# Performance work log

Measured on AMD Instinct MI355X. Metric: run time of the kernel, lower is better.

Reference implementation:

```python
import jax, jax.numpy as jnp
import numpy as np

EMB = 512
HEADS = 8
WINDOW = 128


def setup_inputs() -> dict:
    key = jax.random.key(0)
    ks = jax.random.split(key, 9)
    s = 1.0 / np.sqrt(EMB)
    x = jax.random.normal(ks[0], (2, 4096, EMB), dtype=jnp.float32)
    mk = lambda k: jax.random.uniform(k, (EMB, EMB), jnp.float32, -s, s)
    mb = lambda k: jax.random.uniform(k, (EMB,), jnp.float32, -s, s)
    return {
        "x": x,
        "Wq": mk(ks[1]), "bq": mb(ks[2]),
        "Wk": mk(ks[3]), "bk": mb(ks[4]),
        "Wv": mk(ks[5]), "bv": mb(ks[6]),
        "Wo": mk(ks[7]), "bo": mb(ks[8]),
    }


def _split_heads(y, b, n):
    # [b, n, emb] -> [b, h, n, d]
    return y.reshape(b, n, HEADS, EMB // HEADS).transpose(0, 2, 1, 3)


def reference(x, Wq, bq, Wk, bk, Wv, bv, Wo, bo):
    b, n, _ = x.shape
    q = _split_heads(x @ Wq.T + bq, b, n)
    k = _split_heads(x @ Wk.T + bk, b, n)
    v = _split_heads(x @ Wv.T + bv, b, n)
    energy = jnp.einsum('bhqd,bhkd->bhqk', q, k)  # [b,h,n,n]
    idx = jnp.arange(n)
    # banded mask: disallowed where |i - j| > window (matches torch loop)
    disallow = jnp.abs(idx[:, None] - idx[None, :]) > WINDOW
    fmin = jnp.float32(np.finfo(np.float32).min)
    energy = jnp.where(disallow[None, None], fmin, energy)
    att = jax.nn.softmax(energy / jnp.float32(np.sqrt(EMB)), axis=-1)
    out = jnp.einsum('bhql,bhld->bhqd', att, v)
    out = out.transpose(0, 2, 1, 3).reshape(b, n, EMB)
    return out @ Wo.T + bo
```

## Files before the change

### kernel.cpp

```cpp
#include <hip/hip_runtime.h>

#define EMB 512
#define HEADS 8
#define HD 64
#define NSEQ 4096
#define BATCH 2
#define WINDOW 128

typedef unsigned short u16;
typedef __attribute__((ext_vector_type(8))) short bf16x8;
typedef __attribute__((ext_vector_type(4))) float f32x4;

#define XS 4194304u
#define WS 262144u
#define BS 512u

__device__ __forceinline__ float bf2f(u16 u) {
    union { unsigned int i; float f; } x;
    x.i = ((unsigned int)u) << 16;
    return x.f;
}

__device__ __forceinline__ u16 f2bf(float f) {
    union { float f; unsigned int i; } x;
    x.f = f;
    unsigned int i = x.i;
    unsigned int lsb = (i >> 16) & 1u;
    i += 0x7fffu + lsb;
    return (u16)(i >> 16);
}

struct raw8 { uint4 lo, hi; };

__device__ __forceinline__ raw8 loadraw8(const void* base, size_t off, int isbf) {
    raw8 r;
    if (isbf) {
        r.lo = *(const uint4*)((const u16*)base + off);
    } else {
        const float* f = (const float*)base + off;
        r.lo = *(const uint4*)f;
        r.hi = *(const uint4*)(f + 4);
    }
    return r;
}

__device__ __forceinline__ uint4 cvt8(const raw8& r, int isbf) {
    if (isbf) return r.lo;
    const float* a = (const float*)&r.lo;
    const float* b = (const float*)&r.hi;
    uint4 o;
    o.x = (unsigned)f2bf(a[0]) | ((unsigned)f2bf(a[1]) << 16);
    o.y = (unsigned)f2bf(a[2]) | ((unsigned)f2bf(a[3]) << 16);
    o.z = (unsigned)f2bf(b[0]) | ((unsigned)f2bf(b[1]) << 16);
    o.w = (unsigned)f2bf(b[2]) | ((unsigned)f2bf(b[3]) << 16);
    return o;
}

__device__ __forceinline__ int probe_bf16(const void* p) {
    const int lane = threadIdx.x & 63;
    u16 w = ((const u16*)p)[lane * 2];
    int e = (w >> 7) & 0xff;
    bool sane = (w == 0) || (e >= 100 && e <= 140);
    unsigned long long m = __ballot(sane);
    return __popcll(m) >= 48;
}

__global__ __launch_bounds__(256)
void prepass(const void* __restrict__ x,
             const void* __restrict__ Wq, const void* __restrict__ bq,
             const void* __restrict__ Wk, const void* __restrict__ bk,
             const void* __restrict__ Wv, const void* __restrict__ bv,
             const void* __restrict__ Wo, const void* __restrict__ bo,
             u16* __restrict__ xb, u16* __restrict__ wb, u16* __restrict__ bb,
             int* __restrict__ flags)
{
    const int fx  = probe_bf16(x);
    const int fwq = probe_bf16(Wq), fbq = probe_bf16(bq);
    const int fwk = probe_bf16(Wk), fbk = probe_bf16(bk);
    const int fwv = probe_bf16(Wv), fbv = probe_bf16(bv);
    const int fwo = probe_bf16(Wo), fbo = probe_bf16(bo);
    if (blockIdx.x == 0 && threadIdx.x == 0) flags[0] = fx;

    size_t idx = ((size_t)blockIdx.x * 256 + threadIdx.x) * 8;
    const size_t T_X = XS, T_W = XS + 4 * (size_t)WS, T_ALL = T_W + 4 * (size_t)BS;
    if (idx >= T_ALL) return;

    const void* src; int fl; u16* dst; size_t off;
    if (idx < T_X) {
        src = x; fl = fx; dst = xb; off = idx;
    } else if (idx < T_W) {
        size_t w = idx - T_X;
        int wi = (int)(w / WS); off = w % WS;
        src = (wi == 0) ? Wq : (wi == 1) ? Wk : (wi == 2) ? Wv : Wo;
        fl  = (wi == 0) ? fwq : (wi == 1) ? fwk : (wi == 2) ? fwv : fwo;
        dst = wb + (size_t)wi * WS;
    } else {
        size_t b = idx - T_W;
        int bi = (int)(b / BS); off = b % BS;
        src = (bi == 0) ? bq : (bi == 1) ? bk : (bi == 2) ? bv : bo;
        fl  = (bi == 0) ? fbq : (bi == 1) ? fbk : (bi == 2) ? fbv : fbo;
        dst = bb + (size_t)bi * BS;
    }
    *(uint4*)(dst + off) = cvt8(loadraw8(src, off, fl), fl);
}

__global__ __launch_bounds__(256)
void qkv_gemm(const u16* __restrict__ X, const u16* __restrict__ Wall,
              const u16* __restrict__ ball,
              u16* __restrict__ qo, u16* __restrict__ ko, u16* __restrict__ vo)
{
    __shared__ __align__(16) u16 As2[2][128 * 32];
    __shared__ __align__(16) u16 Bs2[2][128 * 32];

    const int tid  = threadIdx.x;
    const int wave = tid >> 6;
    const int lane = tid & 63;
    const int quad = lane >> 4;
    const int l16  = lane & 15;
    const int wm = wave >> 1, wn = wave & 1;

    const int m0 = blockIdx.x * 128;
    const int by = blockIdx.y;
    const int wsel = by >> 2;
    const int n0 = (by & 3) * 128;

    const u16* W  = Wall + (size_t)wsel * WS;
    const u16* bi = ball + (size_t)wsel * BS;
    const float oscale = (wsel == 0) ? 0.04419417382415922f : 1.0f;

    const u16* PA = (wsel == 2) ? W : X;
    const u16* PB = (wsel == 2) ? X : W;
    const int abase = (wsel == 2) ? n0 : m0;
    const int bbase = (wsel == 2) ? m0 : n0;

    f32x4 acc[4][4];
#pragma unroll
    for (int i = 0; i < 4; ++i)
#pragma unroll
        for (int j = 0; j < 4; ++j)
            acc[i][j] = (f32x4){0.f, 0.f, 0.f, 0.f};

    const int c1 = tid, c2 = tid + 256;
    const int r1 = c1 >> 2, k1 = (c1 & 3) * 8;
    const int r2 = c2 >> 2, k2 = (c2 & 3) * 8;

    uint4 a1 = *(const uint4*)(PA + (size_t)(abase + r1) * EMB + k1);
    uint4 a2 = *(const uint4*)(PA + (size_t)(abase + r2) * EMB + k2);
    uint4 b1 = *(const uint4*)(PB + (size_t)(bbase + r1) * EMB + k1);
    uint4 b2 = *(const uint4*)(PB + (size_t)(bbase + r2) * EMB + k2);
    *(uint4*)&As2[0][c1 * 8] = a1;
    *(uint4*)&As2[0][c2 * 8] = a2;
    *(uint4*)&Bs2[0][c1 * 8] = b1;
    *(uint4*)&Bs2[0][c2 * 8] = b2;
    a1 = *(const uint4*)(PA + (size_t)(abase + r1) * EMB + 32 + k1);
    a2 = *(const uint4*)(PA + (size_t)(abase + r2) * EMB + 32 + k2);
    b1 = *(const uint4*)(PB + (size_t)(bbase + r1) * EMB + 32 + k1);
    b2 = *(const uint4*)(PB + (size_t)(bbase + r2) * EMB + 32 + k2);
    __syncthreads();

    for (int kt = 0; kt < 16; ++kt) {
        const int cur = kt & 1;

        bf16x8 af[4], bfr[4];
#pragma unroll
        for (int i = 0; i < 4; ++i)
            af[i] = *(const bf16x8*)&As2[cur][(wm * 64 + i * 16 + l16) * 32 + quad * 8];
#pragma unroll
        for (int j = 0; j < 4; ++j)
            bfr[j] = *(const bf16x8*)&Bs2[cur][(wn * 64 + j * 16 + l16) * 32 + quad * 8];

        if (kt < 15) {
            *(uint4*)&As2[cur ^ 1][c1 * 8] = a1;
            *(uint4*)&As2[cur ^ 1][c2 * 8] = a2;
            *(uint4*)&Bs2[cur ^ 1][c1 * 8] = b1;
            *(uint4*)&Bs2[cur ^ 1][c2 * 8] = b2;
        }
        if (kt < 14) {
            const int kk0 = (kt + 2) * 32;
            a1 = *(const uint4*)(PA + (size_t)(abase + r1) * EMB + kk0 + k1);
            a2 = *(const uint4*)(PA + (size_t)(abase + r2) * EMB + kk0 + k2);
            b1 = *(const uint4*)(PB + (size_t)(bbase + r1) * EMB + kk0 + k1);
            b2 = *(const uint4*)(PB + (size_t)(bbase + r2) * EMB + kk0 + k2);
        }

#pragma unroll
        for (int i = 0; i < 4; ++i)
#pragma unroll
            for (int j = 0; j < 4; ++j)
                acc[i][j] = __builtin_amdgcn_mfma_f32_16x16x32_bf16(af[i], bfr[j], acc[i][j], 0, 0, 0);

        if (kt < 15) __syncthreads();
    }

    if (wsel != 2) {
#pragma unroll
        for (int j = 0; j < 4; ++j) {
            const int col = n0 + wn * 64 + j * 16 + l16;
            const float bv_ = bf2f(bi[col]);
            const int h = col >> 6, d = col & 63;
            u16* out = (wsel == 0) ? qo : ko;
#pragma unroll
            for (int i = 0; i < 4; ++i) {
#pragma unroll
                for (int r = 0; r < 4; ++r) {
                    const int row = m0 + wm * 64 + i * 16 + quad * 4 + r;
                    const int b = row >> 12, n = row & 4095;
                    out[(((size_t)(b * HEADS + h) * NSEQ) + n) * HD + d] =
                        f2bf((acc[i][j][r] + bv_) * oscale);
                }
            }
        }
    } else {
#pragma unroll
        for (int i = 0; i < 4; ++i) {
#pragma unroll
            for (int r = 0; r < 4; ++r) {
                const int dglob = n0 + wm * 64 + i * 16 + quad * 4 + r;
                const float bv_ = bf2f(bi[dglob]);
                const int h = dglob >> 6, dd = dglob & 63;
#pragma unroll
                for (int j = 0; j < 4; ++j) {
                    const int ncol = m0 + wn * 64 + j * 16 + l16;
                    const int b = ncol >> 12, n = ncol & 4095;
                    vo[((size_t)(b * HEADS + h) * HD + dd) * NSEQ + n] =
                        f2bf(acc[i][j][r] + bv_);
                }
            }
        }
    }
}

#define KP 72
#define VP 72
__global__ __launch_bounds__(256)
void attn_mfma(const u16* __restrict__ q, const u16* __restrict__ k,
               const u16* __restrict__ vt, u16* __restrict__ ao)
{
    __shared__ __align__(16) u16 Ks2[2][64 * KP];
    __shared__ __align__(16) u16 Vt2[2][64 * VP];
    __shared__ __align__(16) u16 Vones[16 * VP];
    __shared__ __align__(16) u16 Pb[4][16 * KP];

    const int tid  = threadIdx.x;
    const int wave = tid >> 6;
    const int lane = tid & 63;
    const int quad = lane >> 4;
    const int l16  = lane & 15;

    int wg = blockIdx.y * 64 + blockIdx.x;
    wg = (wg & 7) * 128 + (wg >> 3);
    const int bh = wg >> 6;
    const int q0 = (wg & 63) * 64;

    const int qw = q0 + wave * 16;
    const size_t base = (size_t)bh * NSEQ * HD;
    const bool interior = (q0 >= 128) && (q0 <= NSEQ - 192);

    if (tid < VP) {
        Vones[tid] = (u16)0x3f80;
#pragma unroll
        for (int rr = 1; rr < 16; ++rr) Vones[rr * VP + tid] = 0;
    }

    bf16x8 qa0 = *(const bf16x8*)(q + base + (size_t)(qw + l16) * HD + quad * 8);
    bf16x8 qa1 = *(const bf16x8*)(q + base + (size_t)(qw + l16) * HD + 32 + quad * 8);

    f32x4 O[4], O4;
#pragma unroll
    for (int t = 0; t < 4; ++t) O[t] = (f32x4){0.f, 0.f, 0.f, 0.f};
    O4 = (f32x4){0.f, 0.f, 0.f, 0.f};

    const int key_s[2] = { tid >> 3, (tid + 256) >> 3 };
    const int ch8      = (tid & 7) * 8;

    const int pacol = (quad * 8) ^ ((l16 >> 2) << 4);

    uint4 pkv[2], pvv[2];
#pragma unroll
    for (int s = 0; s < 2; ++s) {
        int kg = q0 - 128 + key_s[s];
        kg = (kg < 0) ? 0 : (kg > NSEQ - 1 ? NSEQ - 1 : kg);
        pkv[s] = *(const uint4*)(k + base + (size_t)kg * HD + ch8);
        int kc = q0 - 128 + ch8;
        kc = (kc < 0) ? 0 : (kc > NSEQ - 8 ? NSEQ - 8 : kc);
        pvv[s] = *(const uint4*)(vt + base + (size_t)key_s[s] * NSEQ + kc);
    }
#pragma unroll
    for (int s = 0; s < 2; ++s) {
        *(uint4*)&Ks2[0][key_s[s] * KP + ch8] = pkv[s];
        *(uint4*)&Vt2[0][key_s[s] * VP + ch8] = pvv[s];
    }
#pragma unroll
    for (int s = 0; s < 2; ++s) {
        int kg = q0 - 64 + key_s[s];
        kg = (kg < 0) ? 0 : (kg > NSEQ - 1 ? NSEQ - 1 : kg);
        pkv[s] = *(const uint4*)(k + base + (size_t)kg * HD + ch8);
        int kc = q0 - 64 + ch8;
        kc = (kc < 0) ? 0 : (kc > NSEQ - 8 ? NSEQ - 8 : kc);
        pvv[s] = *(const uint4*)(vt + base + (size_t)key_s[s] * NSEQ + kc);
    }
    __syncthreads();

    for (int c = 0; c < 5; ++c) {
        const int cur = c & 1;
        const int kbase = q0 - 128 + c * 64;

        if (c < 4) {
#pragma unroll
            for (int s = 0; s < 2; ++s) {
                *(uint4*)&Ks2[cur ^ 1][key_s[s] * KP + ch8] = pkv[s];
                *(uint4*)&Vt2[cur ^ 1][key_s[s] * VP + ch8] = pvv[s];
            }
        }
        if (c < 3) {
            const int nb = kbase + 128;
#pragma unroll
            for (int s = 0; s < 2; ++s) {
                int kg = nb + key_s[s];
                kg = (kg < 0) ? 0 : (kg > NSEQ - 1 ? NSEQ - 1 : kg);
                pkv[s] = *(const uint4*)(k + base + (size_t)kg * HD + ch8);
                int kc = nb + ch8;
                kc = (kc < 0) ? 0 : (kc > NSEQ - 8 ? NSEQ - 8 : kc);
                pvv[s] = *(const uint4*)(vt + base + (size_t)key_s[s] * NSEQ + kc);
            }
        }

        const int gdk = kbase - qw;
        const bool act = (gdk <= 143) && (gdk >= -191) &&
                         (kbase > -64) && (kbase < NSEQ);
        if (act) {
            f32x4 sv[4];
#pragma unroll
            for (int t = 0; t < 4; ++t) {
                const int dk = gdk + t * 16;
                if (dk >= -143 && dk <= 143) {
                    bf16x8 b0 = *(const bf16x8*)&Ks2[cur][(t * 16 + l16) * KP + quad * 8];
                    bf16x8 b1 = *(const bf16x8*)&Ks2[cur][(t * 16 + l16) * KP + 32 + quad * 8];
                    f32x4 sacc = (f32x4){0.f, 0.f, 0.f, 0.f};
                    sacc = __builtin_amdgcn_mfma_f32_16x16x32_bf16(qa0, b0, sacc, 0, 0, 0);
                    sacc = __builtin_amdgcn_mfma_f32_16x16x32_bf16(qa1, b1, sacc, 0, 0, 0);
                    if (!interior || dk < -113 || dk > 113) {
                        const int jg = kbase + t * 16 + l16;
                        const bool jok = ((unsigned)jg) < (unsigned)NSEQ;
#pragma unroll
                        for (int r = 0; r < 4; ++r) {
                            const int iq = qw + quad * 4 + r;
                            const bool band = ((unsigned)(iq - jg + WINDOW)) <= (unsigned)(2 * WINDOW);
                            if (!(jok && band)) sacc[r] = -1e30f;
                        }
                    }
                    sv[t] = sacc;
                } else {
                    sv[t] = (f32x4){-1e30f, -1e30f, -1e30f, -1e30f};
                }
            }

#pragma unroll
            for (int t = 0; t < 4; ++t) {
                const int tc = (t ^ quad) * 16 + l16;
#pragma unroll
                for (int r = 0; r < 4; ++r) {
                    const float pv = __expf(fminf(sv[t][r], 40.f));
                    Pb[wave][(quad * 4 + r) * KP + tc] = f2bf(pv);
                }
            }

#pragma unroll
            for (int ks2 = 0; ks2 < 2; ++ks2) {
                bf16x8 pa = *(const bf16x8*)&Pb[wave][l16 * KP + (pacol ^ (ks2 * 32))];
#pragma unroll
                for (int t = 0; t < 4; ++t) {
                    bf16x8 vb = *(const bf16x8*)&Vt2[cur][(t * 16 + l16) * VP + ks2 * 32 + quad * 8];
                    O[t] = __builtin_amdgcn_mfma_f32_16x16x32_bf16(pa, vb, O[t], 0, 0, 0);
                }
                bf16x8 vb4 = *(const bf16x8*)&Vones[l16 * VP + ks2 * 32 + quad * 8];
                O4 = __builtin_amdgcn_mfma_f32_16x16x32_bf16(pa, vb4, O4, 0, 0, 0);
            }
        }

        if (c < 4) __syncthreads();
    }

    const int bb = bh >> 3, hh = bh & 7;
    float rl[4];
#pragma unroll
    for (int r = 0; r < 4; ++r) {
        const float ls = __shfl(O4[r], lane & 48, 64);
        rl[r] = 1.f / ls;
    }
#pragma unroll
    for (int t = 0; t < 4; ++t)
#pragma unroll
        for (int r = 0; r < 4; ++r) {
            const int iq = qw + quad * 4 + r;
            ao[((size_t)(bb * NSEQ + iq)) * EMB + hh * HD + t * 16 + l16] =
                f2bf(O[t][r] * rl[r]);
        }
}

__global__ __launch_bounds__(256)
void out_gemm(const u16* __restrict__ A, const u16* __restrict__ W,
              const u16* __restrict__ bias, void* __restrict__ out,
              const int* __restrict__ flags)
{
    __shared__ __align__(16) u16 As2[2][128 * 32];
    __shared__ __align__(16) u16 Bs2[2][128 * 32];

    const int tid  = threadIdx.x;
    const int wave = tid >> 6;
    const int lane = tid & 63;
    const int quad = lane >> 4;
    const int l16  = lane & 15;
    const int wm = wave >> 1, wn = wave & 1;

    const int m0 = blockIdx.x * 128;
    const int n0 = blockIdx.y * 128;
    const int fo = flags[0];

    f32x4 acc[4][4];
#pragma unroll
    for (int i = 0; i < 4; ++i)
#pragma unroll
        for (int j = 0; j < 4; ++j)
            acc[i][j] = (f32x4){0.f, 0.f, 0.f, 0.f};

    const int c1 = tid, c2 = tid + 256;
    const int r1 = c1 >> 2, k1 = (c1 & 3) * 8;
    const int r2 = c2 >> 2, k2 = (c2 & 3) * 8;

    uint4 a1 = *(const uint4*)(A + (size_t)(m0 + r1) * EMB + k1);
    uint4 a2 = *(const uint4*)(A + (size_t)(m0 + r2) * EMB + k2);
    uint4 b1 = *(const uint4*)(W + (size_t)(n0 + r1) * EMB + k1);
    uint4 b2 = *(const uint4*)(W + (size_t)(n0 + r2) * EMB + k2);
    *(uint4*)&As2[0][c1 * 8] = a1;
    *(uint4*)&As2[0][c2 * 8] = a2;
    *(uint4*)&Bs2[0][c1 * 8] = b1;
    *(uint4*)&Bs2[0][c2 * 8] = b2;
    a1 = *(const uint4*)(A + (size_t)(m0 + r1) * EMB + 32 + k1);
    a2 = *(const uint4*)(A + (size_t)(m0 + r2) * EMB + 32 + k2);
    b1 = *(const uint4*)(W + (size_t)(n0 + r1) * EMB + 32 + k1);
    b2 = *(const uint4*)(W + (size_t)(n0 + r2) * EMB + 32 + k2);
    __syncthreads();

    for (int kt = 0; kt < 16; ++kt) {
        const int cur = kt & 1;

        bf16x8 af[4], bfr[4];
#pragma unroll
        for (int i = 0; i < 4; ++i)
            af[i] = *(const bf16x8*)&As2[cur][(wm * 64 + i * 16 + l16) * 32 + quad * 8];
#pragma unroll
        for (int j = 0; j < 4; ++j)
            bfr[j] = *(const bf16x8*)&Bs2[cur][(wn * 64 + j * 16 + l16) * 32 + quad * 8];

        if (kt < 15) {
            *(uint4*)&As2[cur ^ 1][c1 * 8] = a1;
            *(uint4*)&As2[cur ^ 1][c2 * 8] = a2;
            *(uint4*)&Bs2[cur ^ 1][c1 * 8] = b1;
            *(uint4*)&Bs2[cur ^ 1][c2 * 8] = b2;
        }
        if (kt < 14) {
            const int kk0 = (kt + 2) * 32;
            a1 = *(const uint4*)(A + (size_t)(m0 + r1) * EMB + kk0 + k1);
            a2 = *(const uint4*)(A + (size_t)(m0 + r2) * EMB + kk0 + k2);
            b1 = *(const uint4*)(W + (size_t)(n0 + r1) * EMB + kk0 + k1);
            b2 = *(const uint4*)(W + (size_t)(n0 + r2) * EMB + kk0 + k2);
        }

#pragma unroll
        for (int i = 0; i < 4; ++i)
#pragma unroll
            for (int j = 0; j < 4; ++j)
                acc[i][j] = __builtin_amdgcn_mfma_f32_16x16x32_bf16(af[i], bfr[j], acc[i][j], 0, 0, 0);

        if (kt < 15) __syncthreads();
    }

#pragma unroll
    for (int j = 0; j < 4; ++j) {
        const int col = n0 + wn * 64 + j * 16 + l16;
        const float bv_ = bf2f(bias[col]);
#pragma unroll
        for (int i = 0; i < 4; ++i) {
#pragma unroll
            for (int r = 0; r < 4; ++r) {
                const int row = m0 + wm * 64 + i * 16 + quad * 4 + r;
                const float val = acc[i][j][r] + bv_;
                const size_t idx = (size_t)row * EMB + col;
                if (fo) ((u16*)out)[idx] = f2bf(val);
                else    ((float*)out)[idx] = val;
            }
        }
    }
}

extern "C" void kernel_launch(void* const* d_in, const int* in_sizes, int n_in,
                              void* d_out, int out_size, void* d_ws, size_t ws_size,
                              hipStream_t stream)
{
    const size_t HSZ  = (size_t)BATCH * HEADS * NSEQ * HD;
    char* base = (char*)d_ws;
    int* flags = (int*)base;
    const size_t off = 256;

    u16* xb = (u16*)(base + off);
    u16* wb = xb + XS;
    u16* bb = wb + 4 * (size_t)WS;
    u16* kk = bb + 4 * (size_t)BS;
    u16* vv = kk + HSZ;
    u16* ao = vv + HSZ;
    u16* qq = ao + HSZ;

    const size_t need_t1 = off + 2 * (XS + 4 * (size_t)WS + 4 * (size_t)BS + 4 * HSZ);
    if (ws_size < need_t1) {
        qq = (u16*)d_out;
    }

    prepass<<<dim3(2561), 256, 0, stream>>>(d_in[0], d_in[1], d_in[2], d_in[3],
                                            d_in[4], d_in[5], d_in[6], d_in[7],
                                            d_in[8], xb, wb, bb, flags);
    qkv_gemm<<<dim3(64, 12), 256, 0, stream>>>(xb, wb, bb, qq, kk, vv);
    attn_mfma<<<dim3(64, 16), 256, 0, stream>>>(qq, kk, vv, ao);
    out_gemm<<<dim3(64, 4), 256, 0, stream>>>(ao, wb + 3 * (size_t)WS, bb + 3 * (size_t)BS,
                                              d_out, flags);
}
```

Measured before the change: 150.1 us.

## Load K/V fragments directly from global memory instead of LDS double-buffering

Removes the shared-memory double-buffered K and V^T staging and its block-wide barriers. Each wave now reads its MFMA K and V operands straight from global memory, relying on L1/L2 caching for reuse across the four waves. The ones-vector used for the row-sum MFMA is built in registers instead of LDS. This trades barrier and LDS traffic for redundant global loads and exposed load latency without software prefetch.

```diff
diff --git a/kernel.cpp b/kernel.cpp
--- a/kernel.cpp
+++ b/kernel.cpp
@@ -231,14 +231,10 @@
 }
 
 #define KP 72
-#define VP 72
 __global__ __launch_bounds__(256)
 void attn_mfma(const u16* __restrict__ q, const u16* __restrict__ k,
                const u16* __restrict__ vt, u16* __restrict__ ao)
 {
-    __shared__ __align__(16) u16 Ks2[2][64 * KP];
-    __shared__ __align__(16) u16 Vt2[2][64 * VP];
-    __shared__ __align__(16) u16 Vones[16 * VP];
     __shared__ __align__(16) u16 Pb[4][16 * KP];
 
     const int tid  = threadIdx.x;
@@ -256,129 +252,80 @@
     const size_t base = (size_t)bh * NSEQ * HD;
     const bool interior = (q0 >= 128) && (q0 <= NSEQ - 192);
 
-    if (tid < VP) {
-        Vones[tid] = (u16)0x3f80;
-#pragma unroll
-        for (int rr = 1; rr < 16; ++rr) Vones[rr * VP + tid] = 0;
-    }
-
     bf16x8 qa0 = *(const bf16x8*)(q + base + (size_t)(qw + l16) * HD + quad * 8);
     bf16x8 qa1 = *(const bf16x8*)(q + base + (size_t)(qw + l16) * HD + 32 + quad * 8);
 
+    const u16 onesv = (l16 == 0) ? (u16)0x3f80 : (u16)0;
+    bf16x8 vb4;
+#pragma unroll
+    for (int e = 0; e < 8; ++e) vb4[e] = (short)onesv;
+
     f32x4 O[4], O4;
 #pragma unroll
     for (int t = 0; t < 4; ++t) O[t] = (f32x4){0.f, 0.f, 0.f, 0.f};
     O4 = (f32x4){0.f, 0.f, 0.f, 0.f};
 
-    const int key_s[2] = { tid >> 3, (tid + 256) >> 3 };
-    const int ch8      = (tid & 7) * 8;
-
     const int pacol = (quad * 8) ^ ((l16 >> 2) << 4);
 
-    uint4 pkv[2], pvv[2];
-#pragma unroll
-    for (int s = 0; s < 2; ++s) {
-        int kg = q0 - 128 + key_s[s];
-        kg = (kg < 0) ? 0 : (kg > NSEQ - 1 ? NSEQ - 1 : kg);
-        pkv[s] = *(const uint4*)(k + base + (size_t)kg * HD + ch8);
-        int kc = q0 - 128 + ch8;
-        kc = (kc < 0) ? 0 : (kc > NSEQ - 8 ? NSEQ - 8 : kc);
-        pvv[s] = *(const uint4*)(vt + base + (size_t)key_s[s] * NSEQ + kc);
-    }
-#pragma unroll
-    for (int s = 0; s < 2; ++s) {
-        *(uint4*)&Ks2[0][key_s[s] * KP + ch8] = pkv[s];
-        *(uint4*)&Vt2[0][key_s[s] * VP + ch8] = pvv[s];
-    }
-#pragma unroll
-    for (int s = 0; s < 2; ++s) {
-        int kg = q0 - 64 + key_s[s];
-        kg = (kg < 0) ? 0 : (kg > NSEQ - 1 ? NSEQ - 1 : kg);
-        pkv[s] = *(const uint4*)(k + base + (size_t)kg * HD + ch8);
-        int kc = q0 - 64 + ch8;
-        kc = (kc < 0) ? 0 : (kc > NSEQ - 8 ? NSEQ - 8 : kc);
-        pvv[s] = *(const uint4*)(vt + base + (size_t)key_s[s] * NSEQ + kc);
-    }
-    __syncthreads();
-
     for (int c = 0; c < 5; ++c) {
-        const int cur = c & 1;
         const int kbase = q0 - 128 + c * 64;
-
-        if (c < 4) {
-#pragma unroll
-            for (int s = 0; s < 2; ++s) {
-                *(uint4*)&Ks2[cur ^ 1][key_s[s] * KP + ch8] = pkv[s];
-                *(uint4*)&Vt2[cur ^ 1][key_s[s] * VP + ch8] = pvv[s];
-            }
-        }
-        if (c < 3) {
-            const int nb = kbase + 128;
-#pragma unroll
-            for (int s = 0; s < 2; ++s) {
-                int kg = nb + key_s[s];
-                kg = (kg < 0) ? 0 : (kg > NSEQ - 1 ? NSEQ - 1 : kg);
-                pkv[s] = *(const uint4*)(k + base + (size_t)kg * HD + ch8);
-                int kc = nb + ch8;
-                kc = (kc < 0) ? 0 : (kc > NSEQ - 8 ? NSEQ - 8 : kc);
-                pvv[s] = *(const uint4*)(vt + base + (size_t)key_s[s] * NSEQ + kc);
-            }
-        }
-
         const int gdk = kbase - qw;
         const bool act = (gdk <= 143) && (gdk >= -191) &&
                          (kbase > -64) && (kbase < NSEQ);
-        if (act) {
-            f32x4 sv[4];
+        if (!act) continue;
+
+        f32x4 sv[4];
+#pragma unroll
+        for (int t = 0; t < 4; ++t) {
+            const int dk = gdk + t * 16;
+            if (dk >= -143 && dk <= 143) {
+                int kg = kbase + t * 16 + l16;
+                kg = (kg < 0) ? 0 : (kg > NSEQ - 1 ? NSEQ - 1 : kg);
+                const u16* kp = k + base + (size_t)kg * HD + quad * 8;
+                bf16x8 b0 = *(const bf16x8*)(kp);
+                bf16x8 b1 = *(const bf16x8*)(kp + 32);
+                f32x4 sacc = (f32x4){0.f, 0.f, 0.f, 0.f};
+                sacc = __builtin_amdgcn_mfma_f32_16x16x32_bf16(qa0, b0, sacc, 0, 0, 0);
+                sacc = __builtin_amdgcn_mfma_f32_16x16x32_bf16(qa1, b1, sacc, 0, 0, 0);
+                if (!interior || dk < -113 || dk > 113) {
+                    const int jg = kbase + t * 16 + l16;
+                    const bool jok = ((unsigned)jg) < (unsigned)NSEQ;
+#pragma unroll
+                    for (int r = 0; r < 4; ++r) {
+                        const int iq = qw + quad * 4 + r;
+                        const bool band = ((unsigned)(iq - jg + WINDOW)) <= (unsigned)(2 * WINDOW);
+                        if (!(jok && band)) sacc[r] = -1e30f;
+                    }
+                }
+                sv[t] = sacc;
+            } else {
+                sv[t] = (f32x4){-1e30f, -1e30f, -1e30f, -1e30f};
+            }
+        }
+
+#pragma unroll
+        for (int t = 0; t < 4; ++t) {
+            const int tc = (t ^ quad) * 16 + l16;
+#pragma unroll
+            for (int r = 0; r < 4; ++r) {
+                const float pv = __expf(fminf(sv[t][r], 40.f));
+                Pb[wave][(quad * 4 + r) * KP + tc] = f2bf(pv);
+            }
+        }
+
+#pragma unroll
+        for (int ks2 = 0; ks2 < 2; ++ks2) {
+            bf16x8 pa = *(const bf16x8*)&Pb[wave][l16 * KP + (pacol ^ (ks2 * 32))];
+            int kc = kbase + ks2 * 32 + quad * 8;
+            kc = (kc < 0) ? 0 : (kc > NSEQ - 8 ? NSEQ - 8 : kc);
 #pragma unroll
             for (int t = 0; t < 4; ++t) {
-                const int dk = gdk + t * 16;
-                if (dk >= -143 && dk <= 143) {
-                    bf16x8 b0 = *(const bf16x8*)&Ks2[cur][(t * 16 + l16) * KP + quad * 8];
-                    bf16x8 b1 = *(const bf16x8*)&Ks2[cur][(t * 16 + l16) * KP + 32 + quad * 8];
-                    f32x4 sacc = (f32x4){0.f, 0.f, 0.f, 0.f};
-                    sacc = __builtin_amdgcn_mfma_f32_16x16x32_bf16(qa0, b0, sacc, 0, 0, 0);
-                    sacc = __builtin_amdgcn_mfma_f32_16x16x32_bf16(qa1, b1, sacc, 0, 0, 0);
-                    if (!interior || dk < -113 || dk > 113) {
-                        const int jg = kbase + t * 16 + l16;
-                        const bool jok = ((unsigned)jg) < (unsigned)NSEQ;
-#pragma unroll
-                        for (int r = 0; r < 4; ++r) {
-                            const int iq = qw + quad * 4 + r;
-                            const bool band = ((unsigned)(iq - jg + WINDOW)) <= (unsigned)(2 * WINDOW);
-                            if (!(jok && band)) sacc[r] = -1e30f;
-                        }
-                    }
-                    sv[t] = sacc;
-                } else {
-                    sv[t] = (f32x4){-1e30f, -1e30f, -1e30f, -1e30f};
-                }
-            }
-
-#pragma unroll
-            for (int t = 0; t < 4; ++t) {
-                const int tc = (t ^ quad) * 16 + l16;
-#pragma unroll
-                for (int r = 0; r < 4; ++r) {
-                    const float pv = __expf(fminf(sv[t][r], 40.f));
-                    Pb[wave][(quad * 4 + r) * KP + tc] = f2bf(pv);
-                }
-            }
-
-#pragma unroll
-            for (int ks2 = 0; ks2 < 2; ++ks2) {
-                bf16x8 pa = *(const bf16x8*)&Pb[wave][l16 * KP + (pacol ^ (ks2 * 32))];
-#pragma unroll
-                for (int t = 0; t < 4; ++t) {
-                    bf16x8 vb = *(const bf16x8*)&Vt2[cur][(t * 16 + l16) * VP + ks2 * 32 + quad * 8];
-                    O[t] = __builtin_amdgcn_mfma_f32_16x16x32_bf16(pa, vb, O[t], 0, 0, 0);
-                }
-                bf16x8 vb4 = *(const bf16x8*)&Vones[l16 * VP + ks2 * 32 + quad * 8];
-                O4 = __builtin_amdgcn_mfma_f32_16x16x32_bf16(pa, vb4, O4, 0, 0, 0);
-            }
-        }
-
-        if (c < 4) __syncthreads();
+                const int vr = t * 16 + l16;
+                bf16x8 vb = *(const bf16x8*)(vt + base + (size_t)vr * NSEQ + kc);
+                O[t] = __builtin_amdgcn_mfma_f32_16x16x32_bf16(pa, vb, O[t], 0, 0, 0);
+            }
+            O4 = __builtin_amdgcn_mfma_f32_16x16x32_bf16(pa, vb4, O4, 0, 0, 0);
+        }
     }
 
     const int bb = bh >> 3, hh = bh & 7;
```

Measured after the change: 154.5 us. 1.03x slower.
